# Optimization experiments

Measured on AMD Instinct MI355X. Metric: run time of the kernel, lower is better.

## Reference

```python
import jax, jax.numpy as jnp
import numpy as np

B, N, C, H = 8, 1024, 768, 12
DH = C // H


def setup_inputs() -> dict:
    key = jax.random.key(0)
    k1, k2, k3, k4 = jax.random.split(key, 4)
    x = jax.random.normal(k1, (B, N, C), dtype=jnp.float32)
    mask = jax.random.randint(k2, (B, N), 0, 2, dtype=jnp.int32)
    # torch Linear weights stored transposed; build directly as (in, out)
    w_qkv = jax.random.normal(k3, (C, 3 * C), dtype=jnp.float32) * (C ** -0.5)
    w_proj = jax.random.normal(k4, (C, C), dtype=jnp.float32) * (C ** -0.5)
    b_proj = jnp.zeros((C,), dtype=jnp.float32)
    return {"x": x, "mask": mask, "w_qkv": w_qkv, "w_proj": w_proj, "b_proj": b_proj}


def reference(x, mask, w_qkv, w_proj, b_proj):
    scale = DH ** -0.5
    qkv = (x @ w_qkv).reshape(B, N, 3, H, DH)          # (B,N,3,H,Dh)
    q, k, v = jnp.moveaxis(qkv, 2, 0)                  # each (B,N,H,Dh)
    q = q.transpose(0, 2, 1, 3)                        # (B,H,N,Dh)
    k = k.transpose(0, 2, 1, 3)
    v = v.transpose(0, 2, 1, 3)
    attn = jnp.einsum('bhqd,bhkd->bhqk', q, k) * scale  # (B,H,N,N)
    # mask (B,N) masks key positions for all queries/heads
    attn = jnp.where(mask[:, None, None, :] != 0, -jnp.inf, attn)
    attn = jax.nn.softmax(attn, axis=-1)
    out = jnp.einsum('bhqk,bhkd->bhqd', attn, v)        # (B,H,N,Dh)
    out = out.transpose(0, 2, 1, 3).reshape(B, N, C)
    return out @ w_proj + b_proj
```

## Files before the change

### kernel.cpp

```cpp
#include <hip/hip_runtime.h>
#include <cstdint>
#include <cstddef>

#define Bb   8
#define Nn   1024
#define Ccn  768
#define Hh   12
#define DHn  64
#define Mrows (Bb * Nn)
#define N3C  (3 * Ccn)
#define BHn  (Bb * Hh)

typedef __attribute__((ext_vector_type(8))) short bf16x8;
typedef __attribute__((ext_vector_type(4))) float f32x4;

static __device__ __forceinline__ unsigned short f2bf(float f) {
    unsigned int u = __builtin_bit_cast(unsigned int, f);
    return (unsigned short)((u + 0x7FFFu + ((u >> 16) & 1u)) >> 16);
}
static __device__ __forceinline__ float bf2f(unsigned short s) {
    unsigned int u = ((unsigned int)s) << 16;
    return __builtin_bit_cast(float, u);
}
static __device__ __forceinline__ unsigned pack2bf(float a, float b) {
    unsigned ua = __builtin_bit_cast(unsigned, a) + 0x8000u;
    unsigned ub = __builtin_bit_cast(unsigned, b) + 0x8000u;
    return (ua >> 16) | (ub & 0xFFFF0000u);
}
static __device__ __forceinline__ void glds16(const void* g, void* l) {
    __builtin_amdgcn_global_load_lds((const __attribute__((address_space(1))) void*)g,
                                     (__attribute__((address_space(3))) void*)l,
                                     16, 0, 0);
}

__global__ void convert_x_kernel(const float* __restrict__ x,
                                 unsigned short* __restrict__ xb, int n8) {
    int i = blockIdx.x * blockDim.x + threadIdx.x;
    if (i >= n8) return;
    const f32x4* xp = (const f32x4*)x;
    f32x4 a = xp[2 * i], b = xp[2 * i + 1];
    bf16x8 v;
#pragma unroll
    for (int j = 0; j < 4; ++j) {
        v[j]     = (short)f2bf(a[j]);
        v[4 + j] = (short)f2bf(b[j]);
    }
    ((bf16x8*)xb)[i] = v;
}

__global__ void transpose_w_kernel(const float* __restrict__ W,
                                   unsigned short* __restrict__ WT,
                                   int R, int C) {
    __shared__ float tile[32][33];
    const int c0 = blockIdx.x * 32, r0 = blockIdx.y * 32;
    const int tx = threadIdx.x, ty = threadIdx.y;
#pragma unroll
    for (int i = 0; i < 4; ++i)
        tile[ty + i * 8][tx] = W[(size_t)(r0 + ty + i * 8) * C + c0 + tx];
    __syncthreads();
#pragma unroll
    for (int i = 0; i < 4; ++i)
        WT[(size_t)(c0 + ty + i * 8) * R + r0 + tx] = f2bf(tile[tx][ty + i * 8]);
}

__global__ void transpose_v_kernel(const unsigned short* __restrict__ vb,
                                   unsigned short* __restrict__ vtb) {
    __shared__ unsigned short tile[32][34];
    const int bh = blockIdx.z;
    const int d0 = blockIdx.x * 32, n0 = blockIdx.y * 32;
    const int tx = threadIdx.x, ty = threadIdx.y;
    const unsigned short* src = vb + (size_t)bh * Nn * DHn;
    unsigned short* dst = vtb + (size_t)bh * DHn * Nn;
#pragma unroll
    for (int i = 0; i < 4; ++i)
        tile[ty + i * 8][tx] = src[(size_t)(n0 + ty + i * 8) * DHn + d0 + tx];
    __syncthreads();
#pragma unroll
    for (int i = 0; i < 4; ++i)
        dst[(size_t)(d0 + ty + i * 8) * Nn + n0 + tx] = tile[tx][ty + i * 8];
}

__global__ void mask_kernel(const int* __restrict__ mask, float* __restrict__ maskneg) {
    int i = blockIdx.x * 256 + threadIdx.x;
    if (i < Mrows) maskneg[i] = (mask[i] != 0) ? -1.0e9f : 0.0f;
}

__global__ __launch_bounds__(256) void gemm_qkv_kernel(
    const unsigned short* __restrict__ A,
    const unsigned short* __restrict__ BT,
    unsigned short* __restrict__ qkvb) {
    constexpr int K = Ccn;
    const int bm = blockIdx.x, bn = blockIdx.y;
    const int t = threadIdx.x, wv = t >> 6, l = t & 63;
    const int fr = l & 15, quad = l >> 4;
    const int wm = (wv >> 1) * 64, wn = (wv & 1) * 64;
    __shared__ __align__(16) unsigned short As[128 * 32];
    __shared__ __align__(16) unsigned short Bs[128 * 32];
    const f32x4 zero = {0.f, 0.f, 0.f, 0.f};
    f32x4 acc[4][4];
#pragma unroll
    for (int i = 0; i < 4; ++i)
#pragma unroll
        for (int j = 0; j < 4; ++j) acc[i][j] = zero;

    const int srow = wv * 16 + (l >> 2);
    const int scol_dst = (l & 3) * 8;
    const int scol_src = (((l & 3) ^ ((srow >> 1) & 3)) << 3);
    const unsigned short* Ag = A + (size_t)(bm * 128 + srow) * K + scol_src;
    const unsigned short* Bg = BT + (size_t)(bn * 128 + srow) * K + scol_src;
    unsigned short* Al = &As[srow * 32 + scol_dst];
    unsigned short* Bl = &Bs[srow * 32 + scol_dst];
    const int rsw = ((fr >> 1) & 3);

    for (int k0 = 0; k0 < K; k0 += 32) {
        glds16(Ag, Al);
        glds16(Ag + (size_t)64 * K, Al + 64 * 32);
        glds16(Bg, Bl);
        glds16(Bg + (size_t)64 * K, Bl + 64 * 32);
        Ag += 32; Bg += 32;
        __syncthreads();
        bf16x8 af[4], bfv[4];
#pragma unroll
        for (int i = 0; i < 4; ++i)
            af[i] = *(const bf16x8*)&As[(wm + i * 16 + fr) * 32 + ((quad ^ rsw) << 3)];
#pragma unroll
        for (int i = 0; i < 4; ++i)
            bfv[i] = *(const bf16x8*)&Bs[(wn + i * 16 + fr) * 32 + ((quad ^ rsw) << 3)];
#pragma unroll
        for (int i = 0; i < 4; ++i)
#pragma unroll
            for (int j = 0; j < 4; ++j)
                acc[i][j] = __builtin_amdgcn_mfma_f32_16x16x32_bf16(af[i], bfv[j], acc[i][j], 0, 0, 0);
        __syncthreads();
    }
#pragma unroll
    for (int j = 0; j < 4; ++j) {
        int col = bn * 128 + wn + j * 16 + fr;
        int s = col / Ccn;
        int rem = col - s * Ccn;
        int hh = rem >> 6, d = rem & 63;
#pragma unroll
        for (int i = 0; i < 4; ++i) {
#pragma unroll
            for (int r = 0; r < 4; ++r) {
                int row = bm * 128 + wm + i * 16 + quad * 4 + r;
                int b = row >> 10, nq = row & 1023;
                qkvb[((((size_t)s * Bb + b) * Hh + hh) * Nn + nq) * DHn + d] = f2bf(acc[i][j][r]);
            }
        }
    }
}

__global__ __launch_bounds__(256) void gemm_proj_kernel(
    const unsigned short* __restrict__ A,
    const unsigned short* __restrict__ BT,
    const float* __restrict__ bias,
    float* __restrict__ out) {
    constexpr int K = Ccn;
    const int bm = blockIdx.x, bn = blockIdx.y;
    const int t = threadIdx.x, wv = t >> 6, l = t & 63;
    const int fr = l & 15, quad = l >> 4;
    const int wm = (wv >> 1) * 64, wn = (wv & 1) * 64;
    __shared__ __align__(16) unsigned short As[128 * 32];
    __shared__ __align__(16) unsigned short Bs[128 * 32];
    const f32x4 zero = {0.f, 0.f, 0.f, 0.f};
    f32x4 acc[4][4];
#pragma unroll
    for (int i = 0; i < 4; ++i)
#pragma unroll
        for (int j = 0; j < 4; ++j) acc[i][j] = zero;

    const int srow = wv * 16 + (l >> 2);
    const int scol_dst = (l & 3) * 8;
    const int scol_src = (((l & 3) ^ ((srow >> 1) & 3)) << 3);
    const unsigned short* Ag = A + (size_t)(bm * 128 + srow) * K + scol_src;
    const unsigned short* Bg = BT + (size_t)(bn * 128 + srow) * K + scol_src;
    unsigned short* Al = &As[srow * 32 + scol_dst];
    unsigned short* Bl = &Bs[srow * 32 + scol_dst];
    const int rsw = ((fr >> 1) & 3);

    for (int k0 = 0; k0 < K; k0 += 32) {
        glds16(Ag, Al);
        glds16(Ag + (size_t)64 * K, Al + 64 * 32);
        glds16(Bg, Bl);
        glds16(Bg + (size_t)64 * K, Bl + 64 * 32);
        Ag += 32; Bg += 32;
        __syncthreads();
        bf16x8 af[4], bfv[4];
#pragma unroll
        for (int i = 0; i < 4; ++i)
            af[i] = *(const bf16x8*)&As[(wm + i * 16 + fr) * 32 + ((quad ^ rsw) << 3)];
#pragma unroll
        for (int i = 0; i < 4; ++i)
            bfv[i] = *(const bf16x8*)&Bs[(wn + i * 16 + fr) * 32 + ((quad ^ rsw) << 3)];
#pragma unroll
        for (int i = 0; i < 4; ++i)
#pragma unroll
            for (int j = 0; j < 4; ++j)
                acc[i][j] = __builtin_amdgcn_mfma_f32_16x16x32_bf16(af[i], bfv[j], acc[i][j], 0, 0, 0);
        __syncthreads();
    }
#pragma unroll
    for (int j = 0; j < 4; ++j) {
        int col = bn * 128 + wn + j * 16 + fr;
        float bv = bias[col];
#pragma unroll
        for (int i = 0; i < 4; ++i) {
#pragma unroll
            for (int r = 0; r < 4; ++r) {
                int row = bm * 128 + wm + i * 16 + quad * 4 + r;
                out[(size_t)row * Ccn + col] = acc[i][j][r] + bv;
            }
        }
    }
}

__global__ __launch_bounds__(256, 3) void attn_fused(
    const unsigned short* __restrict__ qkvb,
    const unsigned short* __restrict__ vtb,
    const float* __restrict__ maskneg,
    unsigned short* __restrict__ attnb) {
    const int qt = blockIdx.x, h = blockIdx.y, b = blockIdx.z;
    const int t = threadIdx.x, wv = t >> 6, l = t & 63;
    const int fr = l & 15, quad = l >> 4;
    __shared__ __align__(16) unsigned short Ks[64 * 64];
    __shared__ __align__(16) unsigned short VTs[64 * 64];
    __shared__ __align__(16) unsigned short Pbuf[4][16 * 72];
    const size_t bh = (size_t)b * Hh + h;
    const unsigned short* Qg = qkvb + bh * (Nn * DHn);
    const unsigned short* Kg = qkvb + (BHn + bh) * (Nn * DHn);
    const unsigned short* Vg = vtb + bh * (DHn * Nn);
    const float* Mg = maskneg + b * Nn;
    const int q0 = qt * 128 + wv * 32;

    bf16x8 qf[2][2];
#pragma unroll
    for (int g = 0; g < 2; ++g)
#pragma unroll
        for (int c = 0; c < 2; ++c) {
            bf16x8 raw = *(const bf16x8*)&Qg[(size_t)(q0 + g * 16 + fr) * DHn + c * 32 + quad * 8];
            bf16x8 sc;
#pragma unroll
            for (int j = 0; j < 8; ++j)
                sc[j] = (short)f2bf(bf2f((unsigned short)raw[j]) * 0.125f);
            qf[g][c] = sc;
        }
    const f32x4 zero = {0.f, 0.f, 0.f, 0.f};
    f32x4 o[2][4];
    float rs[2] = {0.f, 0.f};
#pragma unroll
    for (int g = 0; g < 2; ++g)
#pragma unroll
        for (int r = 0; r < 4; ++r) o[g][r] = zero;

    const int srow = wv * 8 + (l >> 3);
    const int lincol = (l & 7) * 8;
    const int swzcol = (((l & 7) ^ (srow & 7)) << 3);

    for (int k0 = 0; k0 < Nn; k0 += 64) {
        glds16(&Kg[(size_t)(k0 + srow) * DHn + swzcol], &Ks[srow * 64 + lincol]);
        glds16(&Kg[(size_t)(k0 + srow + 32) * DHn + swzcol], &Ks[(srow + 32) * 64 + lincol]);
        glds16(&Vg[(size_t)srow * Nn + k0 + swzcol], &VTs[srow * 64 + lincol]);
        glds16(&Vg[(size_t)(srow + 32) * Nn + k0 + swzcol], &VTs[(srow + 32) * 64 + lincol]);
        f32x4 ci[4];
#pragma unroll
        for (int kt = 0; kt < 4; ++kt)
            ci[kt] = *(const f32x4*)&Mg[k0 + kt * 16 + quad * 4];
        __syncthreads();

        bf16x8 kf0[4], kf1[4];
#pragma unroll
        for (int kt = 0; kt < 4; ++kt) {
            int rr = kt * 16 + fr, sw = rr & 7;
            kf0[kt] = *(const bf16x8*)&Ks[rr * 64 + ((quad ^ sw) << 3)];
            kf1[kt] = *(const bf16x8*)&Ks[rr * 64 + (((quad + 4) ^ sw) << 3)];
        }
        f32x4 sg[2][4];
#pragma unroll
        for (int g = 0; g < 2; ++g)
#pragma unroll
            for (int kt = 0; kt < 4; ++kt) {
                f32x4 s = __builtin_amdgcn_mfma_f32_16x16x32_bf16(kf0[kt], qf[g][0], ci[kt], 0, 0, 0);
                sg[g][kt] = __builtin_amdgcn_mfma_f32_16x16x32_bf16(kf1[kt], qf[g][1], s, 0, 0, 0);
            }
        bf16x8 vf0[4], vf1[4];
#pragma unroll
        for (int dt = 0; dt < 4; ++dt) {
            int rr = dt * 16 + fr, sw = rr & 7;
            vf0[dt] = *(const bf16x8*)&VTs[rr * 64 + ((quad ^ sw) << 3)];
            vf1[dt] = *(const bf16x8*)&VTs[rr * 64 + (((quad + 4) ^ sw) << 3)];
        }

        unsigned short* Pw = Pbuf[wv];
#pragma unroll
        for (int g = 0; g < 2; ++g) {
#pragma unroll
            for (int kt = 0; kt < 4; ++kt) {
                float p0 = __expf(sg[g][kt][0]);
                float p1 = __expf(sg[g][kt][1]);
                float p2 = __expf(sg[g][kt][2]);
                float p3 = __expf(sg[g][kt][3]);
                rs[g] += (p0 + p1) + (p2 + p3);
                uint2 pk;
                pk.x = pack2bf(p0, p1);
                pk.y = pack2bf(p2, p3);
                *(uint2*)&Pw[fr * 72 + kt * 16 + quad * 4] = pk;
            }
            bf16x8 pa0 = *(const bf16x8*)&Pw[fr * 72 + quad * 8];
            bf16x8 pa1 = *(const bf16x8*)&Pw[fr * 72 + 32 + quad * 8];
#pragma unroll
            for (int dt = 0; dt < 4; ++dt) {
                f32x4 t0 = __builtin_amdgcn_mfma_f32_16x16x32_bf16(pa0, vf0[dt], o[g][dt], 0, 0, 0);
                o[g][dt] = __builtin_amdgcn_mfma_f32_16x16x32_bf16(pa1, vf1[dt], t0, 0, 0, 0);
            }
        }
        __syncthreads();
    }
#pragma unroll
    for (int g = 0; g < 2; ++g) {
        float r2 = rs[g] + __shfl_xor(rs[g], 16, 64);
        float rfull = r2 + __shfl_xor(r2, 32, 64);
        float inv[4];
#pragma unroll
        for (int r = 0; r < 4; ++r) {
            float lv = __shfl(rfull, quad * 4 + r, 64);
            inv[r] = (lv > 0.f) ? 1.0f / lv : 0.f;
        }
#pragma unroll
        for (int dt = 0; dt < 4; ++dt)
#pragma unroll
            for (int r = 0; r < 4; ++r) {
                int q = q0 + g * 16 + quad * 4 + r;
                attnb[((size_t)(b * Nn + q) * Hh + h) * DHn + dt * 16 + fr] = f2bf(o[g][dt][r] * inv[r]);
            }
    }
}

#define OFF_XB     0u
#define OFF_WQKVT  12582912u
#define OFF_WPROJT 16121856u
#define OFF_MASKB  17301504u
#define OFF_QKVB   17334272u
#define OFF_VTB    55083008u
#define OFF_ATTNB  67665920u

extern "C" void kernel_launch(void* const* d_in, const int* in_sizes, int n_in,
                              void* d_out, int out_size, void* d_ws, size_t ws_size,
                              hipStream_t stream) {
    const float* x      = (const float*)d_in[0];
    const int*   mask   = (const int*)d_in[1];
    const float* w_qkv  = (const float*)d_in[2];
    const float* w_proj = (const float*)d_in[3];
    const float* b_proj = (const float*)d_in[4];
    float* out = (float*)d_out;
    char* ws = (char*)d_ws;
    unsigned short* xb     = (unsigned short*)(ws + OFF_XB);
    unsigned short* wqkvT  = (unsigned short*)(ws + OFF_WQKVT);
    unsigned short* wprojT = (unsigned short*)(ws + OFF_WPROJT);
    float*          maskng = (float*)(ws + OFF_MASKB);
    unsigned short* qkvb   = (unsigned short*)(ws + OFF_QKVB);
    unsigned short* vtb    = (unsigned short*)(ws + OFF_VTB);
    unsigned short* attnb  = (unsigned short*)(ws + OFF_ATTNB);

    convert_x_kernel<<<dim3(3072), dim3(256), 0, stream>>>(x, xb, Mrows * Ccn / 8);
    transpose_w_kernel<<<dim3(N3C / 32, Ccn / 32), dim3(32, 8), 0, stream>>>(w_qkv, wqkvT, Ccn, N3C);
    transpose_w_kernel<<<dim3(Ccn / 32, Ccn / 32), dim3(32, 8), 0, stream>>>(w_proj, wprojT, Ccn, Ccn);
    mask_kernel<<<dim3(Mrows / 256), dim3(256), 0, stream>>>(mask, maskng);
    gemm_qkv_kernel<<<dim3(Mrows / 128, N3C / 128), dim3(256), 0, stream>>>(xb, wqkvT, qkvb);
    transpose_v_kernel<<<dim3(DHn / 32, Nn / 32, BHn), dim3(32, 8), 0, stream>>>(
        qkvb + (size_t)2 * BHn * Nn * DHn, vtb);
    attn_fused<<<dim3(Nn / 128, Hh, Bb), dim3(256), 0, stream>>>(qkvb, vtb, maskng, attnb);
    gemm_proj_kernel<<<dim3(Mrows / 128, Ccn / 128), dim3(256), 0, stream>>>(attnb, wprojT, b_proj, out);
}
```

Before: 198.4 us.

## Fuse mask prep into convert, halve proj tile width, widen attention key step

```diff
diff --git a/kernel.cpp b/kernel.cpp
--- a/kernel.cpp
+++ b/kernel.cpp
@@ -33,9 +33,12 @@
                                      16, 0, 0);
 }
 
-__global__ void convert_x_kernel(const float* __restrict__ x,
-                                 unsigned short* __restrict__ xb, int n8) {
+__global__ void convert_x_mask_kernel(const float* __restrict__ x,
+                                      unsigned short* __restrict__ xb,
+                                      const int* __restrict__ mask,
+                                      float* __restrict__ maskneg, int n8) {
     int i = blockIdx.x * blockDim.x + threadIdx.x;
+    if (i < Mrows) maskneg[i] = (mask[i] != 0) ? -1.0e9f : 0.0f;
     if (i >= n8) return;
     const f32x4* xp = (const f32x4*)x;
     f32x4 a = xp[2 * i], b = xp[2 * i + 1];
@@ -78,11 +81,6 @@
 #pragma unroll
     for (int i = 0; i < 4; ++i)
         dst[(size_t)(d0 + ty + i * 8) * Nn + n0 + tx] = tile[tx][ty + i * 8];
-}
-
-__global__ void mask_kernel(const int* __restrict__ mask, float* __restrict__ maskneg) {
-    int i = blockIdx.x * 256 + threadIdx.x;
-    if (i < Mrows) maskneg[i] = (mask[i] != 0) ? -1.0e9f : 0.0f;
 }
 
 __global__ __launch_bounds__(256) void gemm_qkv_kernel(
@@ -160,49 +158,50 @@
     const int bm = blockIdx.x, bn = blockIdx.y;
     const int t = threadIdx.x, wv = t >> 6, l = t & 63;
     const int fr = l & 15, quad = l >> 4;
-    const int wm = (wv >> 1) * 64, wn = (wv & 1) * 64;
+    const int wm = (wv >> 1) * 64, wn = (wv & 1) * 32;
     __shared__ __align__(16) unsigned short As[128 * 32];
-    __shared__ __align__(16) unsigned short Bs[128 * 32];
+    __shared__ __align__(16) unsigned short Bs[64 * 32];
     const f32x4 zero = {0.f, 0.f, 0.f, 0.f};
-    f32x4 acc[4][4];
-#pragma unroll
-    for (int i = 0; i < 4; ++i)
-#pragma unroll
-        for (int j = 0; j < 4; ++j) acc[i][j] = zero;
+    f32x4 acc[4][2];
+#pragma unroll
+    for (int i = 0; i < 4; ++i)
+#pragma unroll
+        for (int j = 0; j < 2; ++j) acc[i][j] = zero;
 
     const int srow = wv * 16 + (l >> 2);
     const int scol_dst = (l & 3) * 8;
     const int scol_src = (((l & 3) ^ ((srow >> 1) & 3)) << 3);
     const unsigned short* Ag = A + (size_t)(bm * 128 + srow) * K + scol_src;
-    const unsigned short* Bg = BT + (size_t)(bn * 128 + srow) * K + scol_src;
     unsigned short* Al = &As[srow * 32 + scol_dst];
-    unsigned short* Bl = &Bs[srow * 32 + scol_dst];
+    const int rB = t >> 2, cB = t & 3;
+    const int bsrc = ((cB ^ ((rB >> 1) & 3)) << 3);
+    const unsigned short* Bg = BT + (size_t)(bn * 64 + rB) * K + bsrc;
+    unsigned short* Bl = &Bs[rB * 32 + cB * 8];
     const int rsw = ((fr >> 1) & 3);
 
     for (int k0 = 0; k0 < K; k0 += 32) {
         glds16(Ag, Al);
         glds16(Ag + (size_t)64 * K, Al + 64 * 32);
         glds16(Bg, Bl);
-        glds16(Bg + (size_t)64 * K, Bl + 64 * 32);
         Ag += 32; Bg += 32;
         __syncthreads();
-        bf16x8 af[4], bfv[4];
+        bf16x8 af[4], bfv[2];
 #pragma unroll
         for (int i = 0; i < 4; ++i)
             af[i] = *(const bf16x8*)&As[(wm + i * 16 + fr) * 32 + ((quad ^ rsw) << 3)];
 #pragma unroll
-        for (int i = 0; i < 4; ++i)
-            bfv[i] = *(const bf16x8*)&Bs[(wn + i * 16 + fr) * 32 + ((quad ^ rsw) << 3)];
-#pragma unroll
-        for (int i = 0; i < 4; ++i)
-#pragma unroll
-            for (int j = 0; j < 4; ++j)
+        for (int j = 0; j < 2; ++j)
+            bfv[j] = *(const bf16x8*)&Bs[(wn + j * 16 + fr) * 32 + ((quad ^ rsw) << 3)];
+#pragma unroll
+        for (int i = 0; i < 4; ++i)
+#pragma unroll
+            for (int j = 0; j < 2; ++j)
                 acc[i][j] = __builtin_amdgcn_mfma_f32_16x16x32_bf16(af[i], bfv[j], acc[i][j], 0, 0, 0);
         __syncthreads();
     }
 #pragma unroll
-    for (int j = 0; j < 4; ++j) {
-        int col = bn * 128 + wn + j * 16 + fr;
+    for (int j = 0; j < 2; ++j) {
+        int col = bn * 64 + wn + j * 16 + fr;
         float bv = bias[col];
 #pragma unroll
         for (int i = 0; i < 4; ++i) {
@@ -220,12 +219,13 @@
     const unsigned short* __restrict__ vtb,
     const float* __restrict__ maskneg,
     unsigned short* __restrict__ attnb) {
-    const int qt = blockIdx.x, h = blockIdx.y, b = blockIdx.z;
+    const int hb = blockIdx.x, qt = blockIdx.y;
+    const int b = hb / Hh, h = hb - b * Hh;
     const int t = threadIdx.x, wv = t >> 6, l = t & 63;
     const int fr = l & 15, quad = l >> 4;
-    __shared__ __align__(16) unsigned short Ks[64 * 64];
-    __shared__ __align__(16) unsigned short VTs[64 * 64];
-    __shared__ __align__(16) unsigned short Pbuf[4][16 * 72];
+    __shared__ __align__(16) unsigned short Ks[2][64 * 64];
+    __shared__ __align__(16) unsigned short VTs[2][64 * 64];
+    __shared__ __align__(16) unsigned short Pbuf[4][2][16 * 72];
     const size_t bh = (size_t)b * Hh + h;
     const unsigned short* Qg = qkvb + bh * (Nn * DHn);
     const unsigned short* Kg = qkvb + (BHn + bh) * (Nn * DHn);
@@ -257,61 +257,69 @@
     const int lincol = (l & 7) * 8;
     const int swzcol = (((l & 7) ^ (srow & 7)) << 3);
 
-    for (int k0 = 0; k0 < Nn; k0 += 64) {
-        glds16(&Kg[(size_t)(k0 + srow) * DHn + swzcol], &Ks[srow * 64 + lincol]);
-        glds16(&Kg[(size_t)(k0 + srow + 32) * DHn + swzcol], &Ks[(srow + 32) * 64 + lincol]);
-        glds16(&Vg[(size_t)srow * Nn + k0 + swzcol], &VTs[srow * 64 + lincol]);
-        glds16(&Vg[(size_t)(srow + 32) * Nn + k0 + swzcol], &VTs[(srow + 32) * 64 + lincol]);
-        f32x4 ci[4];
-#pragma unroll
-        for (int kt = 0; kt < 4; ++kt)
-            ci[kt] = *(const f32x4*)&Mg[k0 + kt * 16 + quad * 4];
-        __syncthreads();
-
-        bf16x8 kf0[4], kf1[4];
-#pragma unroll
-        for (int kt = 0; kt < 4; ++kt) {
-            int rr = kt * 16 + fr, sw = rr & 7;
-            kf0[kt] = *(const bf16x8*)&Ks[rr * 64 + ((quad ^ sw) << 3)];
-            kf1[kt] = *(const bf16x8*)&Ks[rr * 64 + (((quad + 4) ^ sw) << 3)];
-        }
-        f32x4 sg[2][4];
-#pragma unroll
-        for (int g = 0; g < 2; ++g)
+    for (int k0 = 0; k0 < Nn; k0 += 128) {
+#pragma unroll
+        for (int kh = 0; kh < 2; ++kh) {
+            glds16(&Kg[(size_t)(k0 + kh * 64 + srow) * DHn + swzcol], &Ks[kh][srow * 64 + lincol]);
+            glds16(&Kg[(size_t)(k0 + kh * 64 + srow + 32) * DHn + swzcol], &Ks[kh][(srow + 32) * 64 + lincol]);
+            glds16(&Vg[(size_t)srow * Nn + k0 + kh * 64 + swzcol], &VTs[kh][srow * 64 + lincol]);
+            glds16(&Vg[(size_t)(srow + 32) * Nn + k0 + kh * 64 + swzcol], &VTs[kh][(srow + 32) * 64 + lincol]);
+        }
+        f32x4 ci[2][4];
+#pragma unroll
+        for (int kh = 0; kh < 2; ++kh)
+#pragma unroll
+            for (int kt = 0; kt < 4; ++kt)
+                ci[kh][kt] = *(const f32x4*)&Mg[k0 + kh * 64 + kt * 16 + quad * 4];
+        __syncthreads();
+
+#pragma unroll
+        for (int kh = 0; kh < 2; ++kh) {
+            bf16x8 kf0[4], kf1[4];
 #pragma unroll
             for (int kt = 0; kt < 4; ++kt) {
-                f32x4 s = __builtin_amdgcn_mfma_f32_16x16x32_bf16(kf0[kt], qf[g][0], ci[kt], 0, 0, 0);
-                sg[g][kt] = __builtin_amdgcn_mfma_f32_16x16x32_bf16(kf1[kt], qf[g][1], s, 0, 0, 0);
-            }
-        bf16x8 vf0[4], vf1[4];
-#pragma unroll
-        for (int dt = 0; dt < 4; ++dt) {
-            int rr = dt * 16 + fr, sw = rr & 7;
-            vf0[dt] = *(const bf16x8*)&VTs[rr * 64 + ((quad ^ sw) << 3)];
-            vf1[dt] = *(const bf16x8*)&VTs[rr * 64 + (((quad + 4) ^ sw) << 3)];
-        }
-
-        unsigned short* Pw = Pbuf[wv];
-#pragma unroll
-        for (int g = 0; g < 2; ++g) {
-#pragma unroll
-            for (int kt = 0; kt < 4; ++kt) {
-                float p0 = __expf(sg[g][kt][0]);
-                float p1 = __expf(sg[g][kt][1]);
-                float p2 = __expf(sg[g][kt][2]);
-                float p3 = __expf(sg[g][kt][3]);
-                rs[g] += (p0 + p1) + (p2 + p3);
-                uint2 pk;
-                pk.x = pack2bf(p0, p1);
-                pk.y = pack2bf(p2, p3);
-                *(uint2*)&Pw[fr * 72 + kt * 16 + quad * 4] = pk;
-            }
-            bf16x8 pa0 = *(const bf16x8*)&Pw[fr * 72 + quad * 8];
-            bf16x8 pa1 = *(const bf16x8*)&Pw[fr * 72 + 32 + quad * 8];
+                int rr = kt * 16 + fr, sw = rr & 7;
+                kf0[kt] = *(const bf16x8*)&Ks[kh][rr * 64 + ((quad ^ sw) << 3)];
+                kf1[kt] = *(const bf16x8*)&Ks[kh][rr * 64 + (((quad + 4) ^ sw) << 3)];
+            }
+            f32x4 sg[2][4];
+#pragma unroll
+            for (int g = 0; g < 2; ++g)
+#pragma unroll
+                for (int kt = 0; kt < 4; ++kt) {
+                    f32x4 s = __builtin_amdgcn_mfma_f32_16x16x32_bf16(kf0[kt], qf[g][0], ci[kh][kt], 0, 0, 0);
+                    sg[g][kt] = __builtin_amdgcn_mfma_f32_16x16x32_bf16(kf1[kt], qf[g][1], s, 0, 0, 0);
+                }
+            bf16x8 vf0[4], vf1[4];
 #pragma unroll
             for (int dt = 0; dt < 4; ++dt) {
-                f32x4 t0 = __builtin_amdgcn_mfma_f32_16x16x32_bf16(pa0, vf0[dt], o[g][dt], 0, 0, 0);
-                o[g][dt] = __builtin_amdgcn_mfma_f32_16x16x32_bf16(pa1, vf1[dt], t0, 0, 0, 0);
+                int rr = dt * 16 + fr, sw = rr & 7;
+                vf0[dt] = *(const bf16x8*)&VTs[kh][rr * 64 + ((quad ^ sw) << 3)];
+                vf1[dt] = *(const bf16x8*)&VTs[kh][rr * 64 + (((quad + 4) ^ sw) << 3)];
+            }
+
+            unsigned short* Pw = Pbuf[wv][kh];
+#pragma unroll
+            for (int g = 0; g < 2; ++g) {
+#pragma unroll
+                for (int kt = 0; kt < 4; ++kt) {
+                    float p0 = __expf(sg[g][kt][0]);
+                    float p1 = __expf(sg[g][kt][1]);
+                    float p2 = __expf(sg[g][kt][2]);
+                    float p3 = __expf(sg[g][kt][3]);
+                    rs[g] += (p0 + p1) + (p2 + p3);
+                    uint2 pk;
+                    pk.x = pack2bf(p0, p1);
+                    pk.y = pack2bf(p2, p3);
+                    *(uint2*)&Pw[fr * 72 + kt * 16 + quad * 4] = pk;
+                }
+                bf16x8 pa0 = *(const bf16x8*)&Pw[fr * 72 + quad * 8];
+                bf16x8 pa1 = *(const bf16x8*)&Pw[fr * 72 + 32 + quad * 8];
+#pragma unroll
+                for (int dt = 0; dt < 4; ++dt) {
+                    f32x4 t0 = __builtin_amdgcn_mfma_f32_16x16x32_bf16(pa0, vf0[dt], o[g][dt], 0, 0, 0);
+                    o[g][dt] = __builtin_amdgcn_mfma_f32_16x16x32_bf16(pa1, vf1[dt], t0, 0, 0, 0);
+                }
             }
         }
         __syncthreads();
@@ -362,13 +370,12 @@
     unsigned short* vtb    = (unsigned short*)(ws + OFF_VTB);
     unsigned short* attnb  = (unsigned short*)(ws + OFF_ATTNB);
 
-    convert_x_kernel<<<dim3(3072), dim3(256), 0, stream>>>(x, xb, Mrows * Ccn / 8);
+    convert_x_mask_kernel<<<dim3(3072), dim3(256), 0, stream>>>(x, xb, mask, maskng, Mrows * Ccn / 8);
     transpose_w_kernel<<<dim3(N3C / 32, Ccn / 32), dim3(32, 8), 0, stream>>>(w_qkv, wqkvT, Ccn, N3C);
     transpose_w_kernel<<<dim3(Ccn / 32, Ccn / 32), dim3(32, 8), 0, stream>>>(w_proj, wprojT, Ccn, Ccn);
-    mask_kernel<<<dim3(Mrows / 256), dim3(256), 0, stream>>>(mask, maskng);
     gemm_qkv_kernel<<<dim3(Mrows / 128, N3C / 128), dim3(256), 0, stream>>>(xb, wqkvT, qkvb);
     transpose_v_kernel<<<dim3(DHn / 32, Nn / 32, BHn), dim3(32, 8), 0, stream>>>(
         qkvb + (size_t)2 * BHn * Nn * DHn, vtb);
-    attn_fused<<<dim3(Nn / 128, Hh, Bb), dim3(256), 0, stream>>>(qkvb, vtb, maskng, attnb);
-    gemm_proj_kernel<<<dim3(Mrows / 128, Ccn / 128), dim3(256), 0, stream>>>(attnb, wprojT, b_proj, out);
-}
+    attn_fused<<<dim3(BHn, Nn / 128), dim3(256), 0, stream>>>(qkvb, vtb, maskng, attnb);
+    gemm_proj_kernel<<<dim3(Mrows / 128, Ccn / 64), dim3(256), 0, stream>>>(attnb, wprojT, b_proj, out);
+}
```

Result: slower. 208.0 us (+4.8%).
